# Optimization experiments

Hardware: AMD Instinct MI355X
Metric: run time of the kernel (lower is better)

## Reference

```python
import jax, jax.numpy as jnp
import numpy as np


def setup_inputs() -> dict:
    key = jax.random.key(0)
    ks = jax.random.split(key, 8)
    B, C, H, W = 4, 256, 64, 64
    x = jax.random.normal(ks[0], (B, C, H, W), dtype=jnp.float32)
    y = jax.random.normal(ks[1], (B, C, H, W), dtype=jnp.float32)
    s = 1.0 / np.sqrt(C)
    Wq = jax.random.normal(ks[2], (C, C), dtype=jnp.float32) * s
    bq = jax.random.normal(ks[3], (C,), dtype=jnp.float32) * 0.02
    Wk = jax.random.normal(ks[4], (C, C), dtype=jnp.float32) * s
    bk = jax.random.normal(ks[5], (C,), dtype=jnp.float32) * 0.02
    Wv = jax.random.normal(ks[6], (C, C), dtype=jnp.float32) * s
    bv = jax.random.normal(ks[7], (C,), dtype=jnp.float32) * 0.02
    return {"x": x, "y": y, "Wq": Wq, "bq": bq, "Wk": Wk, "bk": bk, "Wv": Wv, "bv": bv}


def reference(x, y, Wq, bq, Wk, bk, Wv, bv):
    B, C, H, W = x.shape
    scale = C ** (-0.5)
    # flatten spatial dims: [B, N, C] with N = H*W
    x_flat = x.reshape(B, C, H * W).transpose(0, 2, 1)
    y_flat = y.reshape(B, C, H * W).transpose(0, 2, 1)
    # linear projections (torch Linear: x @ W.T + b)
    Q = jnp.einsum('bnc,dc->bnd', x_flat, Wq) + bq
    K = jnp.einsum('bnc,dc->bnd', y_flat, Wk) + bk
    V = jnp.einsum('bnc,dc->bnd', y_flat, Wv) + bv
    # single-head full cross-attention
    scores = jnp.einsum('bqd,bkd->bqk', Q, K) * scale  # [B, N, N]
    attn = jax.nn.softmax(scores, axis=-1)
    out = jnp.einsum('bqk,bkd->bqd', attn, V)  # [B, N, C]
    out = out.transpose(0, 2, 1).reshape(B, C, H, W)
    return x + out
```

## Files before the change

kernel.cpp:

```cpp
#include <hip/hip_runtime.h>
#include <stdint.h>

#define BN 4
#define CD 256
#define ND 4096
#define NK 32

typedef unsigned short u16;
typedef short bfrag __attribute__((ext_vector_type(8)));
typedef float ffrag __attribute__((ext_vector_type(4)));

__device__ __forceinline__ float bf2f(u16 u) {
  union { unsigned int i; float f; } v;
  v.i = ((unsigned int)u) << 16;
  return v.f;
}
__device__ __forceinline__ u16 f2bf(float f) {
  union { float f; unsigned int i; } v;
  v.f = f;
  return (u16)((v.i + 0x7FFFu + ((v.i >> 16) & 1u)) >> 16);
}
__device__ __forceinline__ void gload_lds(const u16* g, u16* l) {
  __builtin_amdgcn_global_load_lds(
      (const __attribute__((address_space(1))) void*)g,
      (__attribute__((address_space(3))) void*)l, 16, 0, 0);
}

__global__ __launch_bounds__(256, 2) void k_projQK(
    const float* __restrict__ x, const float* __restrict__ y,
    const float* __restrict__ Wq, const float* __restrict__ Wk,
    const float* __restrict__ bq, const float* __restrict__ bk,
    u16* __restrict__ Qb, u16* __restrict__ Kb) {
  __shared__ alignas(16) u16 As[64][264];
  __shared__ alignas(16) u16 Ws[64][264];
  int m0 = blockIdx.x * 64;
  int z = blockIdx.y;
  int b = m0 >> 12, nsp = m0 & 4095;
  const float* src = (z ? y : x) + (size_t)b * CD * ND;
  const float* Wf = z ? Wk : Wq;
  const float* bias = z ? bk : bq;
  u16* Cd = (z ? Kb : Qb) + (size_t)m0 * CD;
  int t = threadIdx.x, w = t >> 6, l = t & 63;
  int lane16 = l & 15, quad = l >> 4;

#pragma unroll
  for (int it = 0; it < 16; ++it) {
    int idx = it * 256 + t;
    int c = idx >> 4, nj = (idx & 15) * 4;
    float4 v = *(const float4*)(src + (size_t)c * ND + nsp + nj);
    As[nj + 0][c] = f2bf(v.x);
    As[nj + 1][c] = f2bf(v.y);
    As[nj + 2][c] = f2bf(v.z);
    As[nj + 3][c] = f2bf(v.w);
  }
  __syncthreads();

  bfrag af[8];
#pragma unroll
  for (int kc = 0; kc < 8; ++kc)
    af[kc] = *(const bfrag*)&As[w * 16 + lane16][kc * 32 + quad * 8];

  ffrag acc[16];
#pragma unroll
  for (int i = 0; i < 16; ++i) acc[i] = ffrag{0.f, 0.f, 0.f, 0.f};

#pragma unroll
  for (int c4 = 0; c4 < 4; ++c4) {
    if (c4) __syncthreads();
#pragma unroll
    for (int it = 0; it < 16; ++it) {
      int idx = it * 256 + t;
      int row = idx >> 6, col = (idx & 63) * 4;
      float4 v = *(const float4*)(Wf + (size_t)(c4 * 64 + row) * CD + col);
      ushort4 o;
      o.x = f2bf(v.x); o.y = f2bf(v.y); o.z = f2bf(v.z); o.w = f2bf(v.w);
      *(ushort4*)&Ws[row][col] = o;
    }
    __syncthreads();
#pragma unroll
    for (int kc = 0; kc < 8; ++kc)
#pragma unroll
      for (int tt = 0; tt < 4; ++tt) {
        bfrag bfr = *(const bfrag*)&Ws[tt * 16 + lane16][kc * 32 + quad * 8];
        acc[c4 * 4 + tt] =
            __builtin_amdgcn_mfma_f32_16x16x32_bf16(af[kc], bfr, acc[c4 * 4 + tt], 0, 0, 0);
      }
  }
#pragma unroll
  for (int nt = 0; nt < 16; ++nt) {
    int col = nt * 16 + lane16;
    float bcol = bias[col];
#pragma unroll
    for (int r = 0; r < 4; ++r) {
      int rowL = w * 16 + quad * 4 + r;
      Cd[(size_t)rowL * CD + col] = f2bf(acc[nt][r] + bcol);
    }
  }
}

__global__ __launch_bounds__(256, 2) void k_projV(
    const float* __restrict__ y, const float* __restrict__ Wv,
    const float* __restrict__ bv, u16* __restrict__ Vb) {
  __shared__ alignas(16) u16 Bs[64][264];
  __shared__ alignas(16) u16 Ws[64][264];
  int n0s = blockIdx.x * 64;
  int b = blockIdx.y;
  const float* src = y + (size_t)b * CD * ND;
  u16* Cd = Vb + (size_t)b * CD * ND;
  int t = threadIdx.x, w = t >> 6, l = t & 63;
  int lane16 = l & 15, quad = l >> 4;

#pragma unroll
  for (int it = 0; it < 16; ++it) {
    int idx = it * 256 + t;
    int c = idx >> 4, nj = (idx & 15) * 4;
    float4 v = *(const float4*)(src + (size_t)c * ND + n0s + nj);
    Bs[nj + 0][c] = f2bf(v.x);
    Bs[nj + 1][c] = f2bf(v.y);
    Bs[nj + 2][c] = f2bf(v.z);
    Bs[nj + 3][c] = f2bf(v.w);
  }
  __syncthreads();

  bfrag bfr8[8];
#pragma unroll
  for (int kc = 0; kc < 8; ++kc)
    bfr8[kc] = *(const bfrag*)&Bs[w * 16 + lane16][kc * 32 + quad * 8];

  ffrag o[16];
#pragma unroll
  for (int i = 0; i < 16; ++i) o[i] = ffrag{0.f, 0.f, 0.f, 0.f};

#pragma unroll
  for (int c4 = 0; c4 < 4; ++c4) {
    if (c4) __syncthreads();
#pragma unroll
    for (int it = 0; it < 16; ++it) {
      int idx = it * 256 + t;
      int row = idx >> 6, col = (idx & 63) * 4;
      float4 v = *(const float4*)(Wv + (size_t)(c4 * 64 + row) * CD + col);
      ushort4 ov;
      ov.x = f2bf(v.x); ov.y = f2bf(v.y); ov.z = f2bf(v.z); ov.w = f2bf(v.w);
      *(ushort4*)&Ws[row][col] = ov;
    }
    __syncthreads();
#pragma unroll
    for (int kc = 0; kc < 8; ++kc)
#pragma unroll
      for (int mt = 0; mt < 4; ++mt) {
        bfrag af = *(const bfrag*)&Ws[mt * 16 + lane16][kc * 32 + quad * 8];
        o[c4 * 4 + mt] =
            __builtin_amdgcn_mfma_f32_16x16x32_bf16(af, bfr8[kc], o[c4 * 4 + mt], 0, 0, 0);
      }
  }
#pragma unroll
  for (int i = 0; i < 16; ++i) {
    int c4 = i >> 2, mt = i & 3;
#pragma unroll
    for (int r = 0; r < 4; ++r) {
      int d = c4 * 64 + mt * 16 + quad * 4 + r;
      Cd[(size_t)d * ND + n0s + w * 16 + lane16] = f2bf(o[i][r] + bv[d]);
    }
  }
}

union SmemU {
  struct {
    u16 Ks[2][NK][256];
    u16 Vs[2][CD][NK];
    u16 Ps[8][16][40];
  } a;
  u16 ot[CD][136];
};

template <int NS>
__global__ __launch_bounds__(256, 2) void k_attn(
    const u16* __restrict__ Q, const u16* __restrict__ K,
    const u16* __restrict__ Vt, u16* __restrict__ O01,
    u16* __restrict__ O23, float* __restrict__ Lpart) {
  constexpr int NIT = ND / NS / NK;
  __shared__ alignas(16) SmemU sm;
  int b = blockIdx.y, q0 = blockIdx.x * 128, z = blockIdx.z;
  int t = threadIdx.x, w = t >> 6, l = t & 63;
  int lane16 = l & 15, quad = l >> 4;
  const float scale = 0.0625f;

  bfrag qf[2][8];
#pragma unroll
  for (int mi = 0; mi < 2; ++mi) {
    const u16* Qrow =
        Q + ((size_t)b * ND + q0 + (w * 2 + mi) * 16 + lane16) * CD;
#pragma unroll
    for (int kc = 0; kc < 8; ++kc)
      qf[mi][kc] = *(const bfrag*)(Qrow + kc * 32 + quad * 8);
  }

  ffrag o[2][16];
#pragma unroll
  for (int mi = 0; mi < 2; ++mi)
#pragma unroll
    for (int i = 0; i < 16; ++i) o[mi][i] = ffrag{0.f, 0.f, 0.f, 0.f};
  float lsum[2][4] = {{0.f, 0.f, 0.f, 0.f}, {0.f, 0.f, 0.f, 0.f}};

  const u16* Kb = K + ((size_t)b * ND + z * (ND / NS)) * CD;
  const u16* Vb = Vt + (size_t)b * CD * ND + z * (ND / NS);

  auto stage = [&](int kt2) {
    int dbuf = kt2 & 1;
    const u16* Kt = Kb + (size_t)kt2 * NK * CD;
    const u16* Vtt = Vb + kt2 * NK;
#pragma unroll
    for (int p = 0; p < 4; ++p) {
      int r = p * 8 + w * 2 + (l >> 5);
      int j = (l & 31) ^ (r & 7);
      gload_lds(Kt + (size_t)r * CD + j * 8, &sm.a.Ks[dbuf][p * 8 + w * 2][0]);
    }
#pragma unroll
    for (int p = 0; p < 4; ++p) {
      int dd = p * 64 + w * 16 + (l >> 2);
      int j = (l & 3) ^ ((dd >> 1) & 3);
      gload_lds(Vtt + (size_t)dd * ND + j * 8, &sm.a.Vs[dbuf][p * 64 + w * 16][0]);
    }
  };

  stage(0);
  for (int kt = 0; kt < NIT; ++kt) {
    int dbuf = kt & 1;
    __syncthreads();
    if (kt + 1 < NIT) stage(kt + 1);

    ffrag s2[2][2];
#pragma unroll
    for (int mi = 0; mi < 2; ++mi)
#pragma unroll
      for (int tt = 0; tt < 2; ++tt) s2[mi][tt] = ffrag{0.f, 0.f, 0.f, 0.f};
#pragma unroll
    for (int kc = 0; kc < 8; ++kc) {
      bfrag kf0, kf1;
      {
        int r = lane16;
        int cp = (kc * 4 + quad) ^ (r & 7);
        kf0 = *(const bfrag*)&sm.a.Ks[dbuf][r][cp * 8];
        int r1 = 16 + lane16;
        int cp1 = (kc * 4 + quad) ^ (r1 & 7);
        kf1 = *(const bfrag*)&sm.a.Ks[dbuf][r1][cp1 * 8];
      }
#pragma unroll
      for (int mi = 0; mi < 2; ++mi) {
        s2[mi][0] = __builtin_amdgcn_mfma_f32_16x16x32_bf16(qf[mi][kc], kf0,
                                                            s2[mi][0], 0, 0, 0);
        s2[mi][1] = __builtin_amdgcn_mfma_f32_16x16x32_bf16(qf[mi][kc], kf1,
                                                            s2[mi][1], 0, 0, 0);
      }
    }

#pragma unroll
    for (int mi = 0; mi < 2; ++mi)
#pragma unroll
      for (int tt = 0; tt < 2; ++tt)
#pragma unroll
        for (int r = 0; r < 4; ++r) {
          float p = __expf(s2[mi][tt][r] * scale);
          lsum[mi][r] += p;
          sm.a.Ps[w * 2 + mi][quad * 4 + r][tt * 16 + lane16] = f2bf(p);
        }
    bfrag pf0 = *(const bfrag*)&sm.a.Ps[w * 2 + 0][lane16][quad * 8];
    bfrag pf1 = *(const bfrag*)&sm.a.Ps[w * 2 + 1][lane16][quad * 8];

#pragma unroll
    for (int dt = 0; dt < 16; ++dt) {
      int dd = dt * 16 + lane16;
      int cp = quad ^ ((dd >> 1) & 3);
      bfrag vf = *(const bfrag*)&sm.a.Vs[dbuf][dd][cp * 8];
      o[0][dt] = __builtin_amdgcn_mfma_f32_16x16x32_bf16(pf0, vf, o[0][dt], 0, 0, 0);
      o[1][dt] = __builtin_amdgcn_mfma_f32_16x16x32_bf16(pf1, vf, o[1][dt], 0, 0, 0);
    }
  }

#pragma unroll
  for (int mi = 0; mi < 2; ++mi)
#pragma unroll
    for (int r = 0; r < 4; ++r) {
#pragma unroll
      for (int off = 1; off < 16; off <<= 1)
        lsum[mi][r] += __shfl_xor(lsum[mi][r], off, 64);
    }
  if (lane16 == 0) {
#pragma unroll
    for (int mi = 0; mi < 2; ++mi)
#pragma unroll
      for (int r = 0; r < 4; ++r)
        Lpart[((size_t)z * BN + b) * ND + q0 + (w * 2 + mi) * 16 + quad * 4 + r] =
            lsum[mi][r];
  }

  __syncthreads();
#pragma unroll
  for (int mi = 0; mi < 2; ++mi)
#pragma unroll
    for (int dt = 0; dt < 16; ++dt)
#pragma unroll
      for (int r = 0; r < 4; ++r)
        sm.ot[dt * 16 + lane16][(w * 2 + mi) * 16 + quad * 4 + r] =
            f2bf(o[mi][dt][r]);
  __syncthreads();
  const size_t SZc = (size_t)BN * ND * CD;
  u16* Op = ((z < 2) ? O01 : O23) + (size_t)(z & 1) * SZc;
#pragma unroll
  for (int it = 0; it < 16; ++it) {
    int c = it * 256 + t;
    int dd = c >> 4, co = (c & 15) * 8;
    size_t g = ((size_t)b * CD + dd) * ND + q0 + co;
    *(uint4*)(Op + g) = *(const uint4*)&sm.ot[dd][co];
  }
}

template <int NS>
__global__ __launch_bounds__(256) void k_combine(
    const u16* __restrict__ O01, const u16* __restrict__ O23,
    const float* __restrict__ L, const float* __restrict__ x,
    float* __restrict__ out) {
  const size_t SZc = (size_t)BN * ND * CD;
  size_t e = ((size_t)blockIdx.x * 256 + threadIdx.x) * 8;
  int n = (int)(e & (ND - 1));
  int b = (int)(e >> 20);
  float ls[8] = {0, 0, 0, 0, 0, 0, 0, 0};
  float acc[8] = {0, 0, 0, 0, 0, 0, 0, 0};
#pragma unroll
  for (int z = 0; z < NS; ++z) {
    const float* Lr = L + ((size_t)z * BN + b) * ND + n;
    float4 l0 = *(const float4*)(Lr);
    float4 l1 = *(const float4*)(Lr + 4);
    ls[0] += l0.x; ls[1] += l0.y; ls[2] += l0.z; ls[3] += l0.w;
    ls[4] += l1.x; ls[5] += l1.y; ls[6] += l1.z; ls[7] += l1.w;
    const u16* Oz = ((z < 2) ? O01 : O23) + (size_t)(z & 1) * SZc + e;
    union { uint4 q; u16 s[8]; } u;
    u.q = *(const uint4*)Oz;
#pragma unroll
    for (int j = 0; j < 8; ++j) acc[j] += bf2f(u.s[j]);
  }
  float4 x0 = *(const float4*)(x + e);
  float4 x1 = *(const float4*)(x + e + 4);
  float4 r0, r1;
  r0.x = x0.x + acc[0] / ls[0];
  r0.y = x0.y + acc[1] / ls[1];
  r0.z = x0.z + acc[2] / ls[2];
  r0.w = x0.w + acc[3] / ls[3];
  r1.x = x1.x + acc[4] / ls[4];
  r1.y = x1.y + acc[5] / ls[5];
  r1.z = x1.z + acc[6] / ls[6];
  r1.w = x1.w + acc[7] / ls[7];
  *(float4*)(out + e) = r0;
  *(float4*)(out + e + 4) = r1;
}

extern "C" void kernel_launch(void* const* d_in, const int* in_sizes, int n_in,
                              void* d_out, int out_size, void* d_ws, size_t ws_size,
                              hipStream_t stream) {
  const float* x  = (const float*)d_in[0];
  const float* y  = (const float*)d_in[1];
  const float* Wq = (const float*)d_in[2];
  const float* bq = (const float*)d_in[3];
  const float* Wk = (const float*)d_in[4];
  const float* bk = (const float*)d_in[5];
  const float* Wv = (const float*)d_in[6];
  const float* bv = (const float*)d_in[7];
  float* out = (float*)d_out;
  u16* ws = (u16*)d_ws;
  const size_t SZ = (size_t)BN * ND * CD;
  u16* Qb = ws;
  u16* Kb = Qb + SZ;
  u16* Vb = Kb + SZ;
  u16* Ob = Vb + SZ;
  const size_t need4 = 7 * SZ * sizeof(u16) + (size_t)4 * BN * ND * sizeof(float);
  const bool big = ws_size >= need4;
  const int cgrid = (int)(SZ / (256 * 8));

  k_projQK<<<dim3(256, 2), 256, 0, stream>>>(x, y, Wq, Wk, bq, bk, Qb, Kb);
  k_projV<<<dim3(64, 4), 256, 0, stream>>>(y, Wv, bv, Vb);
  if (big) {
    float* Lp = (float*)(Ob + 4 * SZ);
    k_attn<4><<<dim3(ND / 128, BN, 4), 256, 0, stream>>>(Qb, Kb, Vb, Ob,
                                                         Ob + 2 * SZ, Lp);
    k_combine<4><<<dim3(cgrid), 256, 0, stream>>>(Ob, Ob + 2 * SZ, Lp, x, out);
  } else {
    float* Lp = (float*)(Ob + 2 * SZ);
    k_attn<2><<<dim3(ND / 128, BN, 2), 256, 0, stream>>>(Qb, Kb, Vb, Ob, Ob, Lp);
    k_combine<2><<<dim3(cgrid), 256, 0, stream>>>(Ob, Ob, Lp, x, out);
  }
}
```

Baseline: 199.8 us.

## Fuse split-KV combine into attention via last-block atomic counter

Removes the separate combine kernel: each attention block bumps an atomic counter per (query tile, batch), and the last of the NS split blocks reduces the partial outputs and row sums, normalizes, adds the residual and writes the output. The projection kernels' transposed input load changes from float4 per thread to scalar coalesced column loads. This saves a kernel launch and lets the reduction run while other attention blocks are still working, at the cost of a memset, threadfences, and a serialized tail in the last block.

```diff
diff --git a/kernel.cpp b/kernel.cpp
--- a/kernel.cpp
+++ b/kernel.cpp
@@ -43,15 +43,16 @@
   int t = threadIdx.x, w = t >> 6, l = t & 63;
   int lane16 = l & 15, quad = l >> 4;
 
-#pragma unroll
-  for (int it = 0; it < 16; ++it) {
-    int idx = it * 256 + t;
-    int c = idx >> 4, nj = (idx & 15) * 4;
-    float4 v = *(const float4*)(src + (size_t)c * ND + nsp + nj);
-    As[nj + 0][c] = f2bf(v.x);
-    As[nj + 1][c] = f2bf(v.y);
-    As[nj + 2][c] = f2bf(v.z);
-    As[nj + 3][c] = f2bf(v.w);
+  {
+    int u = t & 15, grp = t >> 4;
+#pragma unroll
+    for (int it = 0; it < 16; ++it) {
+      int c = it * 16 + grp;
+      const float* col = src + (size_t)c * ND + nsp;
+#pragma unroll
+      for (int j = 0; j < 4; ++j)
+        As[j * 16 + u][c] = f2bf(col[j * 16 + u]);
+    }
   }
   __syncthreads();
 
@@ -110,15 +111,16 @@
   int t = threadIdx.x, w = t >> 6, l = t & 63;
   int lane16 = l & 15, quad = l >> 4;
 
-#pragma unroll
-  for (int it = 0; it < 16; ++it) {
-    int idx = it * 256 + t;
-    int c = idx >> 4, nj = (idx & 15) * 4;
-    float4 v = *(const float4*)(src + (size_t)c * ND + n0s + nj);
-    Bs[nj + 0][c] = f2bf(v.x);
-    Bs[nj + 1][c] = f2bf(v.y);
-    Bs[nj + 2][c] = f2bf(v.z);
-    Bs[nj + 3][c] = f2bf(v.w);
+  {
+    int u = t & 15, grp = t >> 4;
+#pragma unroll
+    for (int it = 0; it < 16; ++it) {
+      int c = it * 16 + grp;
+      const float* col = src + (size_t)c * ND + n0s;
+#pragma unroll
+      for (int j = 0; j < 4; ++j)
+        Bs[j * 16 + u][c] = f2bf(col[j * 16 + u]);
+    }
   }
   __syncthreads();
 
@@ -171,15 +173,18 @@
     u16 Ps[8][16][40];
   } a;
   u16 ot[CD][136];
+  float ls[128];
 };
 
 template <int NS>
 __global__ __launch_bounds__(256, 2) void k_attn(
     const u16* __restrict__ Q, const u16* __restrict__ K,
-    const u16* __restrict__ Vt, u16* __restrict__ O01,
-    u16* __restrict__ O23, float* __restrict__ Lpart) {
+    const u16* __restrict__ Vt, u16* __restrict__ Opart,
+    float* __restrict__ Lpart, int* __restrict__ cnt,
+    const float* __restrict__ x, float* __restrict__ out) {
   constexpr int NIT = ND / NS / NK;
   __shared__ alignas(16) SmemU sm;
+  __shared__ int lastFlag;
   int b = blockIdx.y, q0 = blockIdx.x * 128, z = blockIdx.z;
   int t = threadIdx.x, w = t >> 6, l = t & 63;
   int lane16 = l & 15, quad = l >> 4;
@@ -305,7 +310,7 @@
             f2bf(o[mi][dt][r]);
   __syncthreads();
   const size_t SZc = (size_t)BN * ND * CD;
-  u16* Op = ((z < 2) ? O01 : O23) + (size_t)(z & 1) * SZc;
+  u16* Op = Opart + (size_t)z * SZc;
 #pragma unroll
   for (int it = 0; it < 16; ++it) {
     int c = it * 256 + t;
@@ -313,45 +318,50 @@
     size_t g = ((size_t)b * CD + dd) * ND + q0 + co;
     *(uint4*)(Op + g) = *(const uint4*)&sm.ot[dd][co];
   }
-}
-
-template <int NS>
-__global__ __launch_bounds__(256) void k_combine(
-    const u16* __restrict__ O01, const u16* __restrict__ O23,
-    const float* __restrict__ L, const float* __restrict__ x,
-    float* __restrict__ out) {
-  const size_t SZc = (size_t)BN * ND * CD;
-  size_t e = ((size_t)blockIdx.x * 256 + threadIdx.x) * 8;
-  int n = (int)(e & (ND - 1));
-  int b = (int)(e >> 20);
-  float ls[8] = {0, 0, 0, 0, 0, 0, 0, 0};
-  float acc[8] = {0, 0, 0, 0, 0, 0, 0, 0};
-#pragma unroll
-  for (int z = 0; z < NS; ++z) {
-    const float* Lr = L + ((size_t)z * BN + b) * ND + n;
-    float4 l0 = *(const float4*)(Lr);
-    float4 l1 = *(const float4*)(Lr + 4);
-    ls[0] += l0.x; ls[1] += l0.y; ls[2] += l0.z; ls[3] += l0.w;
-    ls[4] += l1.x; ls[5] += l1.y; ls[6] += l1.z; ls[7] += l1.w;
-    const u16* Oz = ((z < 2) ? O01 : O23) + (size_t)(z & 1) * SZc + e;
-    union { uint4 q; u16 s[8]; } u;
-    u.q = *(const uint4*)Oz;
-#pragma unroll
-    for (int j = 0; j < 8; ++j) acc[j] += bf2f(u.s[j]);
-  }
-  float4 x0 = *(const float4*)(x + e);
-  float4 x1 = *(const float4*)(x + e + 4);
-  float4 r0, r1;
-  r0.x = x0.x + acc[0] / ls[0];
-  r0.y = x0.y + acc[1] / ls[1];
-  r0.z = x0.z + acc[2] / ls[2];
-  r0.w = x0.w + acc[3] / ls[3];
-  r1.x = x1.x + acc[4] / ls[4];
-  r1.y = x1.y + acc[5] / ls[5];
-  r1.z = x1.z + acc[6] / ls[6];
-  r1.w = x1.w + acc[7] / ls[7];
-  *(float4*)(out + e) = r0;
-  *(float4*)(out + e + 4) = r1;
+
+  __threadfence();
+  __syncthreads();
+  if (t == 0)
+    lastFlag = (atomicAdd(&cnt[blockIdx.x * BN + b], 1) == NS - 1);
+  __syncthreads();
+  if (!lastFlag) return;
+  __threadfence();
+
+  if (t < 128) {
+    float s = 0.f;
+#pragma unroll
+    for (int z2 = 0; z2 < NS; ++z2)
+      s += Lpart[((size_t)z2 * BN + b) * ND + q0 + t];
+    sm.ls[t] = 1.f / s;
+  }
+  __syncthreads();
+#pragma unroll
+  for (int it = 0; it < 16; ++it) {
+    int idx = it * 256 + t;
+    int dd = idx >> 4, qo = (idx & 15) * 8;
+    size_t g = ((size_t)b * CD + dd) * ND + q0 + qo;
+    float av[8] = {0.f, 0.f, 0.f, 0.f, 0.f, 0.f, 0.f, 0.f};
+#pragma unroll
+    for (int z2 = 0; z2 < NS; ++z2) {
+      union { uint4 q4; u16 s[8]; } u;
+      u.q4 = *(const uint4*)(Opart + (size_t)z2 * SZc + g);
+#pragma unroll
+      for (int j = 0; j < 8; ++j) av[j] += bf2f(u.s[j]);
+    }
+    float4 x0 = *(const float4*)(x + g);
+    float4 x1 = *(const float4*)(x + g + 4);
+    float4 r0, r1;
+    r0.x = x0.x + av[0] * sm.ls[qo + 0];
+    r0.y = x0.y + av[1] * sm.ls[qo + 1];
+    r0.z = x0.z + av[2] * sm.ls[qo + 2];
+    r0.w = x0.w + av[3] * sm.ls[qo + 3];
+    r1.x = x1.x + av[4] * sm.ls[qo + 4];
+    r1.y = x1.y + av[5] * sm.ls[qo + 5];
+    r1.z = x1.z + av[6] * sm.ls[qo + 6];
+    r1.w = x1.w + av[7] * sm.ls[qo + 7];
+    *(float4*)(out + g) = r0;
+    *(float4*)(out + g + 4) = r1;
+  }
 }
 
 extern "C" void kernel_launch(void* const* d_in, const int* in_sizes, int n_in,
@@ -372,20 +382,23 @@
   u16* Kb = Qb + SZ;
   u16* Vb = Kb + SZ;
   u16* Ob = Vb + SZ;
-  const size_t need4 = 7 * SZ * sizeof(u16) + (size_t)4 * BN * ND * sizeof(float);
+  const size_t need4 =
+      7 * SZ * sizeof(u16) + (size_t)4 * BN * ND * sizeof(float) + 4096;
   const bool big = ws_size >= need4;
-  const int cgrid = (int)(SZ / (256 * 8));
 
   k_projQK<<<dim3(256, 2), 256, 0, stream>>>(x, y, Wq, Wk, bq, bk, Qb, Kb);
   k_projV<<<dim3(64, 4), 256, 0, stream>>>(y, Wv, bv, Vb);
   if (big) {
     float* Lp = (float*)(Ob + 4 * SZ);
-    k_attn<4><<<dim3(ND / 128, BN, 4), 256, 0, stream>>>(Qb, Kb, Vb, Ob,
-                                                         Ob + 2 * SZ, Lp);
-    k_combine<4><<<dim3(cgrid), 256, 0, stream>>>(Ob, Ob + 2 * SZ, Lp, x, out);
+    int* cnt = (int*)(Lp + (size_t)4 * BN * ND);
+    hipMemsetAsync(cnt, 0, (ND / 128) * BN * sizeof(int), stream);
+    k_attn<4><<<dim3(ND / 128, BN, 4), 256, 0, stream>>>(
+        Qb, Kb, Vb, Ob, Lp, cnt, x, out);
   } else {
     float* Lp = (float*)(Ob + 2 * SZ);
-    k_attn<2><<<dim3(ND / 128, BN, 2), 256, 0, stream>>>(Qb, Kb, Vb, Ob, Ob, Lp);
-    k_combine<2><<<dim3(cgrid), 256, 0, stream>>>(Ob, Ob, Lp, x, out);
-  }
-}
+    int* cnt = (int*)(Lp + (size_t)2 * BN * ND);
+    hipMemsetAsync(cnt, 0, (ND / 128) * BN * sizeof(int), stream);
+    k_attn<2><<<dim3(ND / 128, BN, 2), 256, 0, stream>>>(
+        Qb, Kb, Vb, Ob, Lp, cnt, x, out);
+  }
+}
```

After: 276.1 us. 1.38x slower.
